# Kernel optimization log

Measured on AMD Instinct MI355X. Metric: run time of the kernel, lower is better.

The kernel has to match this reference:

```python
import jax, jax.numpy as jnp
import numpy as np

R_SELF = 0.1  # config.r_self from the 'GENERAL' preset


def setup_inputs() -> dict:
    key = jax.random.key(0)
    k1, k2 = jax.random.split(key)
    N, M, D = 16384, 8192, 128
    x = jax.random.uniform(k1, (N, D), dtype=jnp.float32)
    self_samples = jax.random.uniform(k2, (M, D), dtype=jnp.float32)
    return {"x": x, "self_samples": self_samples}


def _cdist(a, b):
    # Euclidean pairwise distances, same math as torch.cdist(p=2).
    a2 = jnp.sum(a * a, axis=1, keepdims=True)          # [N,1]
    b2 = jnp.sum(b * b, axis=1)[None, :]                # [1,M]
    d2 = a2 + b2 - 2.0 * (a @ b.T)                      # [N,M]
    return jnp.sqrt(jnp.maximum(d2, 0.0))


def reference(x, self_samples):
    # get_anomaly_score: min over self set, shifted by r_self, clamped at 0.
    min_dist_to_self = jnp.min(_cdist(x, self_samples), axis=1)  # [N]
    score = jnp.maximum(min_dist_to_self - R_SELF, 0.0)
    return score
```

## Files before the change

kernel.cpp:

```cpp
#include <hip/hip_runtime.h>


using half_t = _Float16;
typedef _Float16 half8 __attribute__((ext_vector_type(8)));
typedef float floatx16 __attribute__((ext_vector_type(16)));

#define TILE_ELEMS (128 * 128)

__device__ __forceinline__ void async_load16(const void* g, void* l) {
    __builtin_amdgcn_global_load_lds(
        (const __attribute__((address_space(1))) void*)g,
        (__attribute__((address_space(3))) void*)l, 16, 0, 0);
}

__global__ __launch_bounds__(256) void prep_kernel(
    const float* __restrict__ x, const float* __restrict__ self,
    half_t* __restrict__ Aws, half_t* __restrict__ Bws,
    float* __restrict__ b2h, int Atiles)
{
    __shared__ float part[256];
    int tile = blockIdx.x;
    int tid  = threadIdx.x;
    bool isB = tile >= Atiles;
    int bt   = tile - Atiles;
    const float* src = isB ? (self + (size_t)bt * TILE_ELEMS)
                           : (x    + (size_t)tile * TILE_ELEMS);
    half_t* dst = isB ? (Bws + (size_t)bt * TILE_ELEMS)
                      : (Aws + (size_t)tile * TILE_ELEMS);
    float sgn = isB ? 1.f : -1.f;

    int rowt = tid & 127;
    int k8b  = tid >> 7;
    float ss = 0.f;
    #pragma unroll
    for (int i = 0; i < 8; ++i) {
        int k8 = i * 2 + k8b;
        const float4* p = (const float4*)(src + rowt * 128 + k8 * 8);
        float4 f0 = p[0];
        float4 f1 = p[1];
        half8 h;
        h[0] = (half_t)(sgn * f0.x); h[1] = (half_t)(sgn * f0.y);
        h[2] = (half_t)(sgn * f0.z); h[3] = (half_t)(sgn * f0.w);
        h[4] = (half_t)(sgn * f1.x); h[5] = (half_t)(sgn * f1.y);
        h[6] = (half_t)(sgn * f1.z); h[7] = (half_t)(sgn * f1.w);
        *(half8*)(dst + (size_t)(i * 256 + tid) * 8) = h;
        ss += f0.x*f0.x + f0.y*f0.y + f0.z*f0.z + f0.w*f0.w;
        ss += f1.x*f1.x + f1.y*f1.y + f1.z*f1.z + f1.w*f1.w;
    }
    if (isB) {
        part[tid] = ss;
        __syncthreads();
        if (tid < 128)
            b2h[bt * 128 + tid] = 0.5f * (part[tid] + part[tid + 128]);
    }
}

__global__ __launch_bounds__(256, 2) void min_gemm_kernel(
    const half_t* __restrict__ Aws, const half_t* __restrict__ Bws,
    const float* __restrict__ b2h, float* __restrict__ Pmin,
    int Mslice)
{
    __shared__ half_t Bsh[TILE_ELEMS];

    int tid  = threadIdx.x;
    int lane = tid & 63;
    int wid  = tid >> 6;
    int wr   = wid >> 1, wc = wid & 1;
    int ln31 = lane & 31, lh = lane >> 5;

    const half_t* Atile = Aws + (size_t)blockIdx.x * TILE_ELEMS;
    half8 areg[2][8];
    #pragma unroll
    for (int rt = 0; rt < 2; ++rt)
        #pragma unroll
        for (int ki = 0; ki < 8; ++ki) {
            int k8  = ki * 2 + lh;
            int row = wr * 64 + rt * 32 + ln31;
            areg[rt][ki] = *(const half8*)(Atile + (size_t)(k8 * 128 + row) * 8);
        }

    float minacc[2][16];
    #pragma unroll
    for (int rt = 0; rt < 2; ++rt)
        #pragma unroll
        for (int r = 0; r < 16; ++r) minacc[rt][r] = 1e30f;

    int iters = Mslice >> 7;
    int s = blockIdx.y;

    for (int it = 0; it < iters; ++it) {
        const half_t* Bt = Bws + (size_t)(s * iters + it) * TILE_ELEMS;
        __syncthreads();
        #pragma unroll
        for (int j = 0; j < 8; ++j) {
            int seg = wid * 8 + j;
            async_load16(Bt + (size_t)(seg * 64 + lane) * 8,
                         Bsh + (size_t)seg * 512);
        }
        __syncthreads();

        int colbase = s * Mslice + it * 128 + wc * 64 + ln31;
        float b2v0 = b2h[colbase];
        float b2v1 = b2h[colbase + 32];

        floatx16 acc[2][2];
        #pragma unroll
        for (int r = 0; r < 16; ++r) {
            acc[0][0][r] = b2v0; acc[0][1][r] = b2v1;
            acc[1][0][r] = b2v0; acc[1][1][r] = b2v1;
        }

        #pragma unroll
        for (int ki = 0; ki < 8; ++ki) {
            int k8 = ki * 2 + lh;
            half8 bf0 = *(const half8*)(Bsh + (size_t)(k8 * 128 + wc * 64 + ln31) * 8);
            half8 bf1 = *(const half8*)(Bsh + (size_t)(k8 * 128 + wc * 64 + 32 + ln31) * 8);
            acc[0][0] = __builtin_amdgcn_mfma_f32_32x32x16_f16(areg[0][ki], bf0, acc[0][0], 0, 0, 0);
            acc[0][1] = __builtin_amdgcn_mfma_f32_32x32x16_f16(areg[0][ki], bf1, acc[0][1], 0, 0, 0);
            acc[1][0] = __builtin_amdgcn_mfma_f32_32x32x16_f16(areg[1][ki], bf0, acc[1][0], 0, 0, 0);
            acc[1][1] = __builtin_amdgcn_mfma_f32_32x32x16_f16(areg[1][ki], bf1, acc[1][1], 0, 0, 0);
        }

        #pragma unroll
        for (int rt = 0; rt < 2; ++rt)
            #pragma unroll
            for (int r = 0; r < 16; ++r) {
                float v = fminf(acc[rt][0][r], acc[rt][1][r]);
                minacc[rt][r] = fminf(minacc[rt][r], v);
            }
    }

    #pragma unroll
    for (int rt = 0; rt < 2; ++rt)
        #pragma unroll
        for (int r = 0; r < 16; ++r) {
            float v = minacc[rt][r];
            #pragma unroll
            for (int m = 1; m < 32; m <<= 1)
                v = fminf(v, __shfl_xor(v, m, 64));
            if (ln31 == 0) {
                int row = blockIdx.x * 128 + wr * 64 + rt * 32
                        + (r & 3) + 8 * (r >> 2) + 4 * lh;
                Pmin[(size_t)row * 8 + s * 2 + wc] = v;
            }
        }
}

__global__ __launch_bounds__(256) void final_kernel(
    const float* __restrict__ x, const float* __restrict__ Pmin,
    float* __restrict__ out)
{
    int tid  = threadIdx.x;
    int lane = tid & 63, wid = tid >> 6;
    int row  = blockIdx.x * 4 + wid;
    float2 v = ((const float2*)(x + (size_t)row * 128))[lane];
    float ss = v.x * v.x + v.y * v.y;
    #pragma unroll
    for (int m = 1; m < 64; m <<= 1) ss += __shfl_xor(ss, m, 64);
    float p = 1e30f;
    if (lane < 8) p = Pmin[(size_t)row * 8 + lane];
    #pragma unroll
    for (int m = 1; m < 8; m <<= 1) p = fminf(p, __shfl_xor(p, m, 64));
    if (lane == 0) {
        float d2 = ss + 2.f * p;
        float d  = sqrtf(fmaxf(d2, 0.f));
        out[row] = fmaxf(d - 0.1f, 0.f);
    }
}

extern "C" void kernel_launch(void* const* d_in, const int* in_sizes, int n_in,
                              void* d_out, int out_size, void* d_ws, size_t ws_size,
                              hipStream_t stream)
{
    const float* x    = (const float*)d_in[0];
    const float* self = (const float*)d_in[1];
    float* out        = (float*)d_out;

    int N = in_sizes[0] / 128;
    int M = in_sizes[1] / 128;
    int Atiles = N / 128;
    int Btiles = M / 128;

    char* w      = (char*)d_ws;
    half_t* Aws  = (half_t*)w;
    half_t* Bws  = Aws + (size_t)N * 128;
    float*  b2h  = (float*)(w + (size_t)(N + M) * 128 * 2);
    float*  Pmin = b2h + M;

    prep_kernel<<<Atiles + Btiles, 256, 0, stream>>>(x, self, Aws, Bws, b2h, Atiles);

    int Mslice = M / 4;
    dim3 grid(Atiles, 4);
    min_gemm_kernel<<<grid, 256, 0, stream>>>(Aws, Bws, b2h, Pmin, Mslice);

    final_kernel<<<N / 4, 256, 0, stream>>>(x, Pmin, out);
}
```

Baseline: 104.8 us.

## Double-buffer B tiles in LDS and precompute row norms in prep

The min-GEMM kernel now double-buffers B tiles in LDS, prefetching the next tile with async global-to-LDS loads while computing on the current one, and drops one barrier per iteration. The prep kernel also computes the squared norms of x rows, so the final kernel reads a2 and Pmin with one thread per row instead of re-reading x. The extra LDS buffer (64KB per block) may lower occupancy below the two blocks per CU targeted by the launch bounds.

```diff
diff --git a/kernel.cpp b/kernel.cpp
--- a/kernel.cpp
+++ b/kernel.cpp
@@ -16,7 +16,7 @@
 __global__ __launch_bounds__(256) void prep_kernel(
     const float* __restrict__ x, const float* __restrict__ self,
     half_t* __restrict__ Aws, half_t* __restrict__ Bws,
-    float* __restrict__ b2h, int Atiles)
+    float* __restrict__ b2h, float* __restrict__ a2, int Atiles)
 {
     __shared__ float part[256];
     int tile = blockIdx.x;
@@ -47,11 +47,12 @@
         ss += f0.x*f0.x + f0.y*f0.y + f0.z*f0.z + f0.w*f0.w;
         ss += f1.x*f1.x + f1.y*f1.y + f1.z*f1.z + f1.w*f1.w;
     }
-    if (isB) {
-        part[tid] = ss;
-        __syncthreads();
-        if (tid < 128)
-            b2h[bt * 128 + tid] = 0.5f * (part[tid] + part[tid + 128]);
+    part[tid] = ss;
+    __syncthreads();
+    if (tid < 128) {
+        float tot = part[tid] + part[tid + 128];
+        if (isB) b2h[bt * 128 + tid] = 0.5f * tot;
+        else     a2[tile * 128 + tid] = tot;
     }
 }
 
@@ -60,7 +61,7 @@
     const float* __restrict__ b2h, float* __restrict__ Pmin,
     int Mslice)
 {
-    __shared__ half_t Bsh[TILE_ELEMS];
+    __shared__ half_t Bsh[2][TILE_ELEMS];
 
     int tid  = threadIdx.x;
     int lane = tid & 63;
@@ -87,47 +88,71 @@
 
     int iters = Mslice >> 7;
     int s = blockIdx.y;
-
+    const half_t* Bbase = Bws + (size_t)s * iters * TILE_ELEMS;
+
+    #pragma unroll
+    for (int j = 0; j < 8; ++j) {
+        int seg = wid * 8 + j;
+        async_load16(Bbase + (size_t)(seg * 64 + lane) * 8,
+                     &Bsh[0][(size_t)seg * 512]);
+    }
+    __syncthreads();
+
+    float b2v0 = b2h[s * Mslice + wc * 64 + ln31];
+    float b2v1 = b2h[s * Mslice + wc * 64 + 32 + ln31];
+
+    int cur = 0;
     for (int it = 0; it < iters; ++it) {
-        const half_t* Bt = Bws + (size_t)(s * iters + it) * TILE_ELEMS;
+        if (it + 1 < iters) {
+            const half_t* Bt = Bbase + (size_t)(it + 1) * TILE_ELEMS;
+            #pragma unroll
+            for (int j = 0; j < 8; ++j) {
+                int seg = wid * 8 + j;
+                async_load16(Bt + (size_t)(seg * 64 + lane) * 8,
+                             &Bsh[cur ^ 1][(size_t)seg * 512]);
+            }
+        }
+        int nit = (it + 1 < iters) ? it + 1 : it;
+        float nb0 = b2h[s * Mslice + nit * 128 + wc * 64 + ln31];
+        float nb1 = b2h[s * Mslice + nit * 128 + wc * 64 + 32 + ln31];
+
+        floatx16 c0, c1;
+        #pragma unroll
+        for (int r = 0; r < 16; ++r) { c0[r] = b2v0; c1[r] = b2v1; }
+
+        const half_t* Bs = &Bsh[cur][0];
+
+        floatx16 acc00, acc01, acc10, acc11;
+        {
+            int k8 = lh;
+            half8 bf0 = *(const half8*)(Bs + (size_t)(k8 * 128 + wc * 64 + ln31) * 8);
+            half8 bf1 = *(const half8*)(Bs + (size_t)(k8 * 128 + wc * 64 + 32 + ln31) * 8);
+            acc00 = __builtin_amdgcn_mfma_f32_32x32x16_f16(areg[0][0], bf0, c0, 0, 0, 0);
+            acc01 = __builtin_amdgcn_mfma_f32_32x32x16_f16(areg[0][0], bf1, c1, 0, 0, 0);
+            acc10 = __builtin_amdgcn_mfma_f32_32x32x16_f16(areg[1][0], bf0, c0, 0, 0, 0);
+            acc11 = __builtin_amdgcn_mfma_f32_32x32x16_f16(areg[1][0], bf1, c1, 0, 0, 0);
+        }
+        #pragma unroll
+        for (int ki = 1; ki < 8; ++ki) {
+            int k8 = ki * 2 + lh;
+            half8 bf0 = *(const half8*)(Bs + (size_t)(k8 * 128 + wc * 64 + ln31) * 8);
+            half8 bf1 = *(const half8*)(Bs + (size_t)(k8 * 128 + wc * 64 + 32 + ln31) * 8);
+            acc00 = __builtin_amdgcn_mfma_f32_32x32x16_f16(areg[0][ki], bf0, acc00, 0, 0, 0);
+            acc01 = __builtin_amdgcn_mfma_f32_32x32x16_f16(areg[0][ki], bf1, acc01, 0, 0, 0);
+            acc10 = __builtin_amdgcn_mfma_f32_32x32x16_f16(areg[1][ki], bf0, acc10, 0, 0, 0);
+            acc11 = __builtin_amdgcn_mfma_f32_32x32x16_f16(areg[1][ki], bf1, acc11, 0, 0, 0);
+        }
+
+        #pragma unroll
+        for (int r = 0; r < 16; ++r) {
+            minacc[0][r] = fminf(fminf(acc00[r], acc01[r]), minacc[0][r]);
+            minacc[1][r] = fminf(fminf(acc10[r], acc11[r]), minacc[1][r]);
+        }
+
+        b2v0 = nb0; b2v1 = nb1;
+
         __syncthreads();
-        #pragma unroll
-        for (int j = 0; j < 8; ++j) {
-            int seg = wid * 8 + j;
-            async_load16(Bt + (size_t)(seg * 64 + lane) * 8,
-                         Bsh + (size_t)seg * 512);
-        }
-        __syncthreads();
-
-        int colbase = s * Mslice + it * 128 + wc * 64 + ln31;
-        float b2v0 = b2h[colbase];
-        float b2v1 = b2h[colbase + 32];
-
-        floatx16 acc[2][2];
-        #pragma unroll
-        for (int r = 0; r < 16; ++r) {
-            acc[0][0][r] = b2v0; acc[0][1][r] = b2v1;
-            acc[1][0][r] = b2v0; acc[1][1][r] = b2v1;
-        }
-
-        #pragma unroll
-        for (int ki = 0; ki < 8; ++ki) {
-            int k8 = ki * 2 + lh;
-            half8 bf0 = *(const half8*)(Bsh + (size_t)(k8 * 128 + wc * 64 + ln31) * 8);
-            half8 bf1 = *(const half8*)(Bsh + (size_t)(k8 * 128 + wc * 64 + 32 + ln31) * 8);
-            acc[0][0] = __builtin_amdgcn_mfma_f32_32x32x16_f16(areg[0][ki], bf0, acc[0][0], 0, 0, 0);
-            acc[0][1] = __builtin_amdgcn_mfma_f32_32x32x16_f16(areg[0][ki], bf1, acc[0][1], 0, 0, 0);
-            acc[1][0] = __builtin_amdgcn_mfma_f32_32x32x16_f16(areg[1][ki], bf0, acc[1][0], 0, 0, 0);
-            acc[1][1] = __builtin_amdgcn_mfma_f32_32x32x16_f16(areg[1][ki], bf1, acc[1][1], 0, 0, 0);
-        }
-
-        #pragma unroll
-        for (int rt = 0; rt < 2; ++rt)
-            #pragma unroll
-            for (int r = 0; r < 16; ++r) {
-                float v = fminf(acc[rt][0][r], acc[rt][1][r]);
-                minacc[rt][r] = fminf(minacc[rt][r], v);
-            }
+        cur ^= 1;
     }
 
     #pragma unroll
@@ -147,25 +172,18 @@
 }
 
 __global__ __launch_bounds__(256) void final_kernel(
-    const float* __restrict__ x, const float* __restrict__ Pmin,
+    const float* __restrict__ a2, const float* __restrict__ Pmin,
     float* __restrict__ out)
 {
-    int tid  = threadIdx.x;
-    int lane = tid & 63, wid = tid >> 6;
-    int row  = blockIdx.x * 4 + wid;
-    float2 v = ((const float2*)(x + (size_t)row * 128))[lane];
-    float ss = v.x * v.x + v.y * v.y;
-    #pragma unroll
-    for (int m = 1; m < 64; m <<= 1) ss += __shfl_xor(ss, m, 64);
-    float p = 1e30f;
-    if (lane < 8) p = Pmin[(size_t)row * 8 + lane];
-    #pragma unroll
-    for (int m = 1; m < 8; m <<= 1) p = fminf(p, __shfl_xor(p, m, 64));
-    if (lane == 0) {
-        float d2 = ss + 2.f * p;
-        float d  = sqrtf(fmaxf(d2, 0.f));
-        out[row] = fmaxf(d - 0.1f, 0.f);
-    }
+    int row = blockIdx.x * 256 + threadIdx.x;
+    const float4* pp = (const float4*)(Pmin + (size_t)row * 8);
+    float4 p0 = pp[0];
+    float4 p1 = pp[1];
+    float p = fminf(fminf(fminf(p0.x, p0.y), fminf(p0.z, p0.w)),
+                    fminf(fminf(p1.x, p1.y), fminf(p1.z, p1.w)));
+    float d2 = a2[row] + 2.f * p;
+    float d  = sqrtf(fmaxf(d2, 0.f));
+    out[row] = fmaxf(d - 0.1f, 0.f);
 }
 
 extern "C" void kernel_launch(void* const* d_in, const int* in_sizes, int n_in,
@@ -186,12 +204,13 @@
     half_t* Bws  = Aws + (size_t)N * 128;
     float*  b2h  = (float*)(w + (size_t)(N + M) * 128 * 2);
     float*  Pmin = b2h + M;
-
-    prep_kernel<<<Atiles + Btiles, 256, 0, stream>>>(x, self, Aws, Bws, b2h, Atiles);
+    float*  a2   = Pmin + (size_t)N * 8;
+
+    prep_kernel<<<Atiles + Btiles, 256, 0, stream>>>(x, self, Aws, Bws, b2h, a2, Atiles);
 
     int Mslice = M / 4;
     dim3 grid(Atiles, 4);
     min_gemm_kernel<<<grid, 256, 0, stream>>>(Aws, Bws, b2h, Pmin, Mslice);
 
-    final_kernel<<<N / 4, 256, 0, stream>>>(x, Pmin, out);
-}
+    final_kernel<<<N / 256, 256, 0, stream>>>(a2, Pmin, out);
+}
```

After: 102.3 us. 2.4% less time.
